# Performance work log

Measured on AMD Instinct MI355X. Metric: run time of the kernel, lower is better.

The kernel has to match this reference:

```python
import jax, jax.numpy as jnp
import numpy as np

EMBED_DIM = 1024
NUM_HEADS = 16
HEAD_DIM = EMBED_DIM // NUM_HEADS
BSZ, TGT, SRC = 4, 2048, 2048


def setup_inputs() -> dict:
    key = jax.random.key(0)
    ks = jax.random.split(key, 8)
    s = EMBED_DIM ** -0.5  # keep activations O(1)
    return {
        "query": jax.random.normal(ks[0], (BSZ, TGT, EMBED_DIM), jnp.float32),
        "key": jax.random.normal(ks[1], (BSZ, SRC, EMBED_DIM), jnp.float32),
        "key_padding_mask": jnp.ones((BSZ, SRC), jnp.float32),
        "Wq": jax.random.normal(ks[2], (EMBED_DIM, EMBED_DIM), jnp.float32) * s,
        "bq": jnp.zeros((EMBED_DIM,), jnp.float32),
        "Wk": jax.random.normal(ks[3], (EMBED_DIM, EMBED_DIM), jnp.float32) * s,
        "bk": jnp.zeros((EMBED_DIM,), jnp.float32),
        "Wv": jax.random.normal(ks[4], (EMBED_DIM, EMBED_DIM), jnp.float32) * s,
        "bv": jnp.zeros((EMBED_DIM,), jnp.float32),
        "Wo": jax.random.normal(ks[5], (EMBED_DIM, EMBED_DIM), jnp.float32) * s,
        "bo": jnp.zeros((EMBED_DIM,), jnp.float32),
    }


def _split_heads(x, bsz, seqlen):
    # [b, s, e] -> [b, h, s, d]
    return x.reshape(bsz, seqlen, NUM_HEADS, HEAD_DIM).transpose(0, 2, 1, 3)


def reference(query, key, key_padding_mask, Wq, bq, Wk, bk, Wv, bv, Wo, bo):
    bsz, src_len, embed_dim = key.shape
    tgt_len = query.shape[1]
    scaling = HEAD_DIM ** -0.5

    q = (query @ Wq.T + bq) * scaling                # [b, t, e]
    k = key @ Wk.T + bk                              # [b, s, e]
    v = key @ Wv.T + bv                              # [b, s, e]

    qh = _split_heads(q, bsz, tgt_len)               # [b, h, t, d]
    kh = _split_heads(k, bsz, src_len)               # [b, h, s, d]
    vh = _split_heads(v, bsz, src_len)               # [b, h, s, d]

    scores = jnp.einsum('bhtd,bhsd->bhts', qh, kh)   # [b, h, t, s]

    # _expand_mask: additive mask, 0 where mask==1, finfo.min where mask==0
    inv = 1.0 - key_padding_mask.astype(scores.dtype)
    neg = jnp.finfo(scores.dtype).min
    add_mask = jnp.where(inv.astype(bool), neg, inv)  # [b, s]
    scores = scores + add_mask[:, None, None, :]

    probs = jax.nn.softmax(scores, axis=-1)          # dropout p=0 / eval -> identity

    out = jnp.einsum('bhts,bhsd->bhtd', probs, vh)   # [b, h, t, d]
    out = out.transpose(0, 2, 1, 3).reshape(bsz, tgt_len, embed_dim)
    return out @ Wo.T + bo
```

## Files before the change

kernel.cpp:

```cpp
#include <hip/hip_runtime.h>

typedef unsigned short u16;
typedef __attribute__((ext_vector_type(8))) short bf16x8;
typedef __attribute__((ext_vector_type(4))) float f32x4;
typedef __attribute__((ext_vector_type(16))) float f32x16;

#define LOG2E 1.44269504088896f

__device__ inline u16 f2b(float f) {
  union { float f; unsigned u; } x; x.f = f;
  unsigned r = x.u + 0x7fffu + ((x.u >> 16) & 1u);
  return (u16)(r >> 16);
}

__device__ inline void gload_lds16(const void* g, void* l) {
  __builtin_amdgcn_global_load_lds(
      (__attribute__((address_space(1))) void*)(g),
      (__attribute__((address_space(3))) void*)(l), 16, 0, 0);
}

__device__ inline unsigned cvtpk_bf16(float lo, float hi_) {
  unsigned r;
  asm("v_cvt_pk_bf16_f32 %0, %1, %2" : "=v"(r) : "v"(lo), "v"(hi_));
  return r;
}
__device__ inline float exp2_hw(float x) { return __builtin_amdgcn_exp2f(x); }

__global__ __launch_bounds__(256) void cvt_all(
    const float* __restrict__ q, const float* __restrict__ k,
    const float* __restrict__ wq, const float* __restrict__ wk,
    const float* __restrict__ wv, const float* __restrict__ wo,
    u16* __restrict__ qb, u16* __restrict__ kb,
    u16* __restrict__ wqb, u16* __restrict__ wkb,
    u16* __restrict__ wvb, u16* __restrict__ wob) {
  int b = blockIdx.x;
  const float* in;
  u16* out;
  if (b < 8192) {
    in = q; out = qb;
  } else if (b < 16384) {
    in = k; out = kb; b -= 8192;
  } else {
    const int w = (b - 16384) >> 10;
    b = (b - 16384) & 1023;
    in = (w == 0) ? wq : (w == 1) ? wk : (w == 2) ? wv : wo;
    out = (w == 0) ? wqb : (w == 1) ? wkb : (w == 2) ? wvb : wob;
  }
  const int i = b * 256 + threadIdx.x;
  const float4 v = ((const float4*)in)[i];
  union { u16 s[4]; uint2 u; } o;
  o.s[0] = f2b(v.x); o.s[1] = f2b(v.y); o.s[2] = f2b(v.z); o.s[3] = f2b(v.w);
  ((uint2*)out)[i] = o.u;
}

template <int OUTMODE>
__global__ __launch_bounds__(256) void gemm_bt2(
    const u16* __restrict__ A, const u16* __restrict__ W,
    const float* __restrict__ bias, void* __restrict__ Cout,
    int M, int N, int K, float alpha) {
  __shared__ __align__(16) u16 lA[2][128 * 32];
  __shared__ __align__(16) u16 lW[2][128 * 32];
  const int tid = threadIdx.x, lane = tid & 63, wid = tid >> 6;
  const int wr = wid >> 1, wc = wid & 1;
  const int fr = lane & 15, fq = lane >> 4;
  const size_t abase = (size_t)blockIdx.x * 128 * K;
  const size_t wbase = (size_t)blockIdx.y * 128 * K;

  f32x4 acc[4][4];
#pragma unroll
  for (int i = 0; i < 4; ++i)
#pragma unroll
    for (int j = 0; j < 4; ++j) acc[i][j] = (f32x4){0.f, 0.f, 0.f, 0.f};

#define GSTAGE(bufi, kt)                                                          \
  do {                                                                            \
    _Pragma("unroll")                                                             \
    for (int is = 0; is < 2; ++is) {                                              \
      const int idx = is * 256 + tid;                                             \
      const int r = idx >> 2, c8 = (idx & 3) << 3;                                \
      gload_lds16(A + abase + (size_t)r * K + (kt) + c8, lA[bufi] + idx * 8);     \
      gload_lds16(W + wbase + (size_t)r * K + (kt) + c8, lW[bufi] + idx * 8);     \
    }                                                                             \
  } while (0)

  GSTAGE(0, 0);
  __syncthreads();

  int buf = 0;
  for (int kt = 0; kt < K; kt += 32) {
    if (kt + 32 < K) GSTAGE(buf ^ 1, kt + 32);
    bf16x8 af[4], wf[4];
#pragma unroll
    for (int m = 0; m < 4; ++m)
      af[m] = *(const bf16x8*)&lA[buf][(wr * 64 + m * 16 + fr) * 32 + fq * 8];
#pragma unroll
    for (int n = 0; n < 4; ++n)
      wf[n] = *(const bf16x8*)&lW[buf][(wc * 64 + n * 16 + fr) * 32 + fq * 8];
#pragma unroll
    for (int m = 0; m < 4; ++m)
#pragma unroll
      for (int n = 0; n < 4; ++n)
        acc[m][n] = __builtin_amdgcn_mfma_f32_16x16x32_bf16(af[m], wf[n], acc[m][n], 0, 0, 0);
    __syncthreads();
    buf ^= 1;
  }
#undef GSTAGE

  const int row0 = blockIdx.x * 128 + wr * 64 + fq * 4;
  const int col0 = blockIdx.y * 128 + wc * 64 + fr;
#pragma unroll
  for (int n = 0; n < 4; ++n) {
    const int col = col0 + n * 16;
    const float bb = bias[col];
#pragma unroll
    for (int m = 0; m < 4; ++m) {
#pragma unroll
      for (int r = 0; r < 4; ++r) {
        const int row = row0 + m * 16 + r;
        const float v = (acc[m][n][r] + bb) * alpha;
        if (OUTMODE == 1)
          ((float*)Cout)[(size_t)row * N + col] = v;
        else
          ((u16*)Cout)[(size_t)row * N + col] = f2b(v);
      }
    }
  }
}

__global__ __launch_bounds__(256) void gemm_kv(
    const u16* __restrict__ A, const u16* __restrict__ Wk,
    const u16* __restrict__ Wv, const float* __restrict__ bk,
    const float* __restrict__ bv, u16* __restrict__ Kout,
    u16* __restrict__ Vtout, int K) {
  __shared__ __align__(16) u16 lA[2][128 * 32];
  __shared__ __align__(16) u16 lW[2][128 * 32];
  const int tid = threadIdx.x, lane = tid & 63, wid = tid >> 6;
  const int wr = wid >> 1, wc = wid & 1;
  const int fr = lane & 15, fq = lane >> 4;
  const int isV = blockIdx.y >> 3, ny = blockIdx.y & 7;
  const u16* W = isV ? Wv : Wk;
  const float* bias = isV ? bv : bk;
  const size_t abase = (size_t)blockIdx.x * 128 * K;
  const size_t wbase = (size_t)ny * 128 * K;

  f32x4 acc[4][4];
#pragma unroll
  for (int i = 0; i < 4; ++i)
#pragma unroll
    for (int j = 0; j < 4; ++j) acc[i][j] = (f32x4){0.f, 0.f, 0.f, 0.f};

#define GSTAGE(bufi, kt)                                                          \
  do {                                                                            \
    _Pragma("unroll")                                                             \
    for (int is = 0; is < 2; ++is) {                                              \
      const int idx = is * 256 + tid;                                             \
      const int r = idx >> 2, c8 = (idx & 3) << 3;                                \
      gload_lds16(A + abase + (size_t)r * K + (kt) + c8, lA[bufi] + idx * 8);     \
      gload_lds16(W + wbase + (size_t)r * K + (kt) + c8, lW[bufi] + idx * 8);     \
    }                                                                             \
  } while (0)

  GSTAGE(0, 0);
  __syncthreads();

  int buf = 0;
  for (int kt = 0; kt < K; kt += 32) {
    if (kt + 32 < K) GSTAGE(buf ^ 1, kt + 32);
    bf16x8 af[4], wf[4];
#pragma unroll
    for (int m = 0; m < 4; ++m)
      af[m] = *(const bf16x8*)&lA[buf][(wr * 64 + m * 16 + fr) * 32 + fq * 8];
#pragma unroll
    for (int n = 0; n < 4; ++n)
      wf[n] = *(const bf16x8*)&lW[buf][(wc * 64 + n * 16 + fr) * 32 + fq * 8];
#pragma unroll
    for (int m = 0; m < 4; ++m)
#pragma unroll
      for (int n = 0; n < 4; ++n)
        acc[m][n] = __builtin_amdgcn_mfma_f32_16x16x32_bf16(af[m], wf[n], acc[m][n], 0, 0, 0);
    __syncthreads();
    buf ^= 1;
  }
#undef GSTAGE

  if (isV) {
    const int bI = blockIdx.x >> 4;
    const int srow0 = ((blockIdx.x * 128) & 2047) + wr * 64 + fq * 4;
    const int col0 = ny * 128 + wc * 64 + fr;
#pragma unroll
    for (int n = 0; n < 4; ++n) {
      const int col = col0 + n * 16;
      const float bb = bias[col];
      const int h = col >> 6, dl = col & 63;
      u16* vrow = Vtout + ((size_t)((bI * 16 + h) * 64 + dl)) * 2048;
#pragma unroll
      for (int m = 0; m < 4; ++m) {
        const int s = srow0 + m * 16;
        const int x = s & 15;
        const int pos = (((s & 63) >> 4) * 2 + ((x >> 2) & 1)) * 8 + ((x & 3) | ((x & 8) >> 1));
        union { u16 s4[4]; uint2 u; } w;
#pragma unroll
        for (int r = 0; r < 4; ++r) w.s4[r] = f2b(acc[m][n][r] + bb);
        *(uint2*)&vrow[(s >> 6) * 64 + pos] = w.u;
      }
    }
  } else {
    const int row0 = blockIdx.x * 128 + wr * 64 + fq * 4;
    const int col0 = ny * 128 + wc * 64 + fr;
#pragma unroll
    for (int n = 0; n < 4; ++n) {
      const int col = col0 + n * 16;
      const float bb = bias[col];
#pragma unroll
      for (int m = 0; m < 4; ++m) {
#pragma unroll
        for (int r = 0; r < 4; ++r) {
          const int row = row0 + m * 16 + r;
          Kout[(size_t)row * 1024 + col] = f2b(acc[m][n][r] + bb);
        }
      }
    }
  }
}

__global__ __launch_bounds__(512, 4) void flash16(
    const u16* __restrict__ Qb, const u16* __restrict__ Kb,
    const u16* __restrict__ Vt, const float* __restrict__ mask,
    u16* __restrict__ Ob) {
  __shared__ __align__(16) u16 Kl[2][4096];
  __shared__ __align__(16) u16 Vl[2][4096];
  __shared__ unsigned long long bml[32];
  __shared__ float lbuf[8][32];

  const int f = blockIdx.x;
  const int xcd = f & 7, i = f >> 3;
  const int bh = xcd * 8 + (i >> 3);
  const int qt = i & 7;
  const int b = bh >> 4, h = bh & 15;
  const int tid = threadIdx.x, lane = tid & 63, wid = tid >> 6;
  const int l31 = lane & 31, hi = lane >> 5;
  const int qrow0 = qt * 256 + wid * 32;

  bf16x8 qf[4];
  {
    const u16* qp = Qb + ((size_t)(b * 2048 + qrow0 + l31)) * 1024 + h * 64;
#pragma unroll
    for (int dc = 0; dc < 4; ++dc) qf[dc] = *(const bf16x8*)(qp + dc * 16 + hi * 8);
  }

  const u16* kbase = Kb + ((size_t)(b * 2048)) * 1024 + h * 64;
  const u16* vbase = Vt + ((size_t)(bh * 64)) * 2048;
  const float* mrow = mask + b * 2048;

  const int l31s = tid & 31, his = (tid >> 5) & 1, mid = (tid >> 6) & 3,
            top = (tid >> 8) & 1;
  const int koff = (top * 32 + l31s) * 1024 + (mid * 2 + his) * 8;
  const int voff = (top * 32 + l31s) * 2048 + (mid * 2 + his) * 8;

  f32x16 o0 = {}, o1 = {};
  float l_r = 0.f;

#define STAGE(bufi, tt)                               \
  do {                                                \
    const u16* kb_t = kbase + (size_t)(tt) * 65536;   \
    const u16* vb_t = vbase + (tt) * 64;              \
    gload_lds16(kb_t + koff, &Kl[bufi][tid * 8]);     \
    gload_lds16(vb_t + voff, &Vl[bufi][tid * 8]);     \
  } while (0)

  STAGE(0, 0);

#pragma unroll
  for (int tt = 0; tt < 4; ++tt) {
    const int tile = wid * 4 + tt;
    const unsigned long long bmv = __ballot(mrow[tile * 64 + lane] == 1.0f);
    if (lane == 0) bml[tile] = bmv;
  }
  __syncthreads();

  const unsigned mflags =
      (unsigned)__ballot(lane < 32 && bml[lane] != ~0ull);

  for (int t = 0; t < 32; ++t) {
    const int cur = t & 1;
    if (t + 1 < 32) STAGE(cur ^ 1, t + 1);

    const u16* Kc = Kl[cur];
    const u16* Vc = Vl[cur];

#pragma unroll
    for (int n = 0; n < 2; ++n) {
      f32x16 acc = {};
#pragma unroll
      for (int dc = 0; dc < 4; ++dc) {
        const bf16x8 kf = *(const bf16x8*)&Kc[(n * 4 + dc) * 512 + lane * 8];
        acc = __builtin_amdgcn_mfma_f32_32x32x16_bf16(kf, qf[dc], acc, 0, 0, 0);
      }

#pragma unroll
      for (int reg = 0; reg < 16; ++reg) acc[reg] = exp2_hw(acc[reg]);

      if (mflags & (1u << t)) {
        const unsigned long long bm = bml[t];
#pragma unroll
        for (int reg = 0; reg < 16; ++reg) {
          const int k = n * 32 + (reg & 3) + 8 * (reg >> 2) + 4 * hi;
          if (!((bm >> k) & 1)) acc[reg] = 0.f;
        }
      }

      {
        float s0a = (acc[0] + acc[1]) + (acc[2] + acc[3]);
        float s1a = (acc[4] + acc[5]) + (acc[6] + acc[7]);
        float s2a = (acc[8] + acc[9]) + (acc[10] + acc[11]);
        float s3a = (acc[12] + acc[13]) + (acc[14] + acc[15]);
        l_r += (s0a + s1a) + (s2a + s3a);
      }

      bf16x8 pa0, pa1;
      {
        union { unsigned u[4]; bf16x8 v; } pk;
#pragma unroll
        for (int j = 0; j < 4; ++j) pk.u[j] = cvtpk_bf16(acc[2 * j], acc[2 * j + 1]);
        pa0 = pk.v;
#pragma unroll
        for (int j = 0; j < 4; ++j) pk.u[j] = cvtpk_bf16(acc[8 + 2 * j], acc[9 + 2 * j]);
        pa1 = pk.v;
      }

      {
        const bf16x8 v00 = *(const bf16x8*)&Vc[(0 * 4 + n * 2 + 0) * 512 + lane * 8];
        const bf16x8 v01 = *(const bf16x8*)&Vc[(0 * 4 + n * 2 + 1) * 512 + lane * 8];
        o0 = __builtin_amdgcn_mfma_f32_32x32x16_bf16(pa0, v00, o0, 0, 0, 0);
        o0 = __builtin_amdgcn_mfma_f32_32x32x16_bf16(pa1, v01, o0, 0, 0, 0);
      }
      {
        const bf16x8 v10 = *(const bf16x8*)&Vc[(1 * 4 + n * 2 + 0) * 512 + lane * 8];
        const bf16x8 v11 = *(const bf16x8*)&Vc[(1 * 4 + n * 2 + 1) * 512 + lane * 8];
        o1 = __builtin_amdgcn_mfma_f32_32x32x16_bf16(pa0, v10, o1, 0, 0, 0);
        o1 = __builtin_amdgcn_mfma_f32_32x32x16_bf16(pa1, v11, o1, 0, 0, 0);
      }
    }

    __syncthreads();
  }
#undef STAGE

  const float l_tot = l_r + __shfl_xor(l_r, 32);
  const float linv = 1.0f / l_tot;
  if (!hi) lbuf[wid][l31] = linv;
  __builtin_amdgcn_wave_barrier();
  float lv[16];
#pragma unroll
  for (int reg = 0; reg < 16; ++reg)
    lv[reg] = lbuf[wid][(reg & 3) + 8 * (reg >> 2) + 4 * hi];

  u16* ob = Ob + ((size_t)(b * 2048 + qrow0)) * 1024 + h * 64 + l31;
#pragma unroll
  for (int reg = 0; reg < 16; ++reg) {
    const int q = (reg & 3) + 8 * (reg >> 2) + 4 * hi;
    ob[(size_t)q * 1024] = f2b(o0[reg] * lv[reg]);
    ob[(size_t)q * 1024 + 32] = f2b(o1[reg] * lv[reg]);
  }
}

extern "C" void kernel_launch(void* const* d_in, const int* in_sizes, int n_in,
                              void* d_out, int out_size, void* d_ws, size_t ws_size,
                              hipStream_t stream) {
  const float* query = (const float*)d_in[0];
  const float* keyin = (const float*)d_in[1];
  const float* maskp = (const float*)d_in[2];
  const float* Wq = (const float*)d_in[3];
  const float* bq = (const float*)d_in[4];
  const float* Wk = (const float*)d_in[5];
  const float* bk = (const float*)d_in[6];
  const float* Wv = (const float*)d_in[7];
  const float* bv = (const float*)d_in[8];
  const float* Wo = (const float*)d_in[9];
  const float* bo = (const float*)d_in[10];

  char* ws = (char*)d_ws;
  const size_t ACT = (size_t)8192 * 1024 * 2;
  const size_t WMAT = (size_t)1024 * 1024 * 2;
  u16* qbf = (u16*)(ws);
  u16* kbf = (u16*)(ws + ACT);
  u16* wqb = (u16*)(ws + 2 * ACT);
  u16* wkb = (u16*)(ws + 2 * ACT + WMAT);
  u16* wvb = (u16*)(ws + 2 * ACT + 2 * WMAT);
  u16* wob = (u16*)(ws + 2 * ACT + 3 * WMAT);
  u16* Qb  = (u16*)(ws + 2 * ACT + 4 * WMAT);
  u16* Kb  = (u16*)(ws + 3 * ACT + 4 * WMAT);
  u16* Vt = qbf;
  u16* attnb = kbf;

  cvt_all<<<20480, 256, 0, stream>>>(query, keyin, Wq, Wk, Wv, Wo,
                                     qbf, kbf, wqb, wkb, wvb, wob);

  dim3 gg(64, 8);
  gemm_bt2<0><<<gg, 256, 0, stream>>>(qbf, wqb, bq, Qb, 8192, 1024, 1024, 0.125f * LOG2E);
  gemm_kv<<<dim3(64, 16), 256, 0, stream>>>(kbf, wkb, wvb, bk, bv, Kb, Vt, 1024);

  flash16<<<512, 512, 0, stream>>>(Qb, Kb, Vt, maskp, attnb);

  gemm_bt2<1><<<gg, 256, 0, stream>>>(attnb, wob, bo, d_out, 8192, 1024, 1024, 1.0f);
}
```

Measured before the change: 203.6 us.

## Fuse Q, K, V projections into one launch and deepen GEMM K-tile to 64

Merges the separate Q projection GEMM and the K/V GEMM into a single 64x24-block launch that picks its input, weight, bias and output per blockIdx.y. Vt now goes to a dedicated workspace region because qbf is still being read by the Q blocks in the same launch. Both GEMMs now stage 64-wide K slices (double-buffered, 64 KB LDS), which halves the barrier count per tile. The cost is more LDS per block, which may lower occupancy, and the workspace must be large enough for the extra buffer.

```diff
diff --git a/kernel.cpp b/kernel.cpp
--- a/kernel.cpp
+++ b/kernel.cpp
@@ -53,13 +53,12 @@
   ((uint2*)out)[i] = o.u;
 }
 
-template <int OUTMODE>
-__global__ __launch_bounds__(256) void gemm_bt2(
+__global__ __launch_bounds__(256) void gemm_o(
     const u16* __restrict__ A, const u16* __restrict__ W,
-    const float* __restrict__ bias, void* __restrict__ Cout,
-    int M, int N, int K, float alpha) {
-  __shared__ __align__(16) u16 lA[2][128 * 32];
-  __shared__ __align__(16) u16 lW[2][128 * 32];
+    const float* __restrict__ bias, float* __restrict__ Cout,
+    int K) {
+  __shared__ __align__(16) u16 lA[2][128 * 64];
+  __shared__ __align__(16) u16 lW[2][128 * 64];
   const int tid = threadIdx.x, lane = tid & 63, wid = tid >> 6;
   const int wr = wid >> 1, wc = wid & 1;
   const int fr = lane & 15, fq = lane >> 4;
@@ -75,11 +74,11 @@
 #define GSTAGE(bufi, kt)                                                          \
   do {                                                                            \
     _Pragma("unroll")                                                             \
-    for (int is = 0; is < 2; ++is) {                                              \
-      const int idx = is * 256 + tid;                                             \
-      const int r = idx >> 2, c8 = (idx & 3) << 3;                                \
-      gload_lds16(A + abase + (size_t)r * K + (kt) + c8, lA[bufi] + idx * 8);     \
-      gload_lds16(W + wbase + (size_t)r * K + (kt) + c8, lW[bufi] + idx * 8);     \
+    for (int is = 0; is < 4; ++is) {                                              \
+      const int c = is * 256 + tid;                                               \
+      const int r = c >> 3, c8 = (c & 7) << 3;                                    \
+      gload_lds16(A + abase + (size_t)r * K + (kt) + c8, lA[bufi] + c * 8);       \
+      gload_lds16(W + wbase + (size_t)r * K + (kt) + c8, lW[bufi] + c * 8);       \
     }                                                                             \
   } while (0)
 
@@ -87,20 +86,23 @@
   __syncthreads();
 
   int buf = 0;
-  for (int kt = 0; kt < K; kt += 32) {
-    if (kt + 32 < K) GSTAGE(buf ^ 1, kt + 32);
-    bf16x8 af[4], wf[4];
-#pragma unroll
-    for (int m = 0; m < 4; ++m)
-      af[m] = *(const bf16x8*)&lA[buf][(wr * 64 + m * 16 + fr) * 32 + fq * 8];
-#pragma unroll
-    for (int n = 0; n < 4; ++n)
-      wf[n] = *(const bf16x8*)&lW[buf][(wc * 64 + n * 16 + fr) * 32 + fq * 8];
-#pragma unroll
-    for (int m = 0; m < 4; ++m)
+  for (int kt = 0; kt < K; kt += 64) {
+    if (kt + 64 < K) GSTAGE(buf ^ 1, kt + 64);
+#pragma unroll
+    for (int kk = 0; kk < 2; ++kk) {
+      bf16x8 af[4], wf[4];
+#pragma unroll
+      for (int m = 0; m < 4; ++m)
+        af[m] = *(const bf16x8*)&lA[buf][(wr * 64 + m * 16 + fr) * 64 + kk * 32 + fq * 8];
 #pragma unroll
       for (int n = 0; n < 4; ++n)
-        acc[m][n] = __builtin_amdgcn_mfma_f32_16x16x32_bf16(af[m], wf[n], acc[m][n], 0, 0, 0);
+        wf[n] = *(const bf16x8*)&lW[buf][(wc * 64 + n * 16 + fr) * 64 + kk * 32 + fq * 8];
+#pragma unroll
+      for (int m = 0; m < 4; ++m)
+#pragma unroll
+        for (int n = 0; n < 4; ++n)
+          acc[m][n] = __builtin_amdgcn_mfma_f32_16x16x32_bf16(af[m], wf[n], acc[m][n], 0, 0, 0);
+    }
     __syncthreads();
     buf ^= 1;
   }
@@ -117,29 +119,28 @@
 #pragma unroll
       for (int r = 0; r < 4; ++r) {
         const int row = row0 + m * 16 + r;
-        const float v = (acc[m][n][r] + bb) * alpha;
-        if (OUTMODE == 1)
-          ((float*)Cout)[(size_t)row * N + col] = v;
-        else
-          ((u16*)Cout)[(size_t)row * N + col] = f2b(v);
-      }
-    }
-  }
-}
-
-__global__ __launch_bounds__(256) void gemm_kv(
-    const u16* __restrict__ A, const u16* __restrict__ Wk,
-    const u16* __restrict__ Wv, const float* __restrict__ bk,
-    const float* __restrict__ bv, u16* __restrict__ Kout,
+        Cout[(size_t)row * 1024 + col] = acc[m][n][r] + bb;
+      }
+    }
+  }
+}
+
+__global__ __launch_bounds__(256) void gemm_qkv(
+    const u16* __restrict__ qA, const u16* __restrict__ kA,
+    const u16* __restrict__ Wq, const u16* __restrict__ Wk,
+    const u16* __restrict__ Wv, const float* __restrict__ bq,
+    const float* __restrict__ bk, const float* __restrict__ bv,
+    u16* __restrict__ Qout, u16* __restrict__ Kout,
     u16* __restrict__ Vtout, int K) {
-  __shared__ __align__(16) u16 lA[2][128 * 32];
-  __shared__ __align__(16) u16 lW[2][128 * 32];
+  __shared__ __align__(16) u16 lA[2][128 * 64];
+  __shared__ __align__(16) u16 lW[2][128 * 64];
   const int tid = threadIdx.x, lane = tid & 63, wid = tid >> 6;
   const int wr = wid >> 1, wc = wid & 1;
   const int fr = lane & 15, fq = lane >> 4;
-  const int isV = blockIdx.y >> 3, ny = blockIdx.y & 7;
-  const u16* W = isV ? Wv : Wk;
-  const float* bias = isV ? bv : bk;
+  const int path = blockIdx.y >> 3, ny = blockIdx.y & 7;
+  const u16* A = (path == 0) ? qA : kA;
+  const u16* W = (path == 0) ? Wq : (path == 1) ? Wk : Wv;
+  const float* bias = (path == 0) ? bq : (path == 1) ? bk : bv;
   const size_t abase = (size_t)blockIdx.x * 128 * K;
   const size_t wbase = (size_t)ny * 128 * K;
 
@@ -152,11 +153,11 @@
 #define GSTAGE(bufi, kt)                                                          \
   do {                                                                            \
     _Pragma("unroll")                                                             \
-    for (int is = 0; is < 2; ++is) {                                              \
-      const int idx = is * 256 + tid;                                             \
-      const int r = idx >> 2, c8 = (idx & 3) << 3;                                \
-      gload_lds16(A + abase + (size_t)r * K + (kt) + c8, lA[bufi] + idx * 8);     \
-      gload_lds16(W + wbase + (size_t)r * K + (kt) + c8, lW[bufi] + idx * 8);     \
+    for (int is = 0; is < 4; ++is) {                                              \
+      const int c = is * 256 + tid;                                               \
+      const int r = c >> 3, c8 = (c & 7) << 3;                                    \
+      gload_lds16(A + abase + (size_t)r * K + (kt) + c8, lA[bufi] + c * 8);       \
+      gload_lds16(W + wbase + (size_t)r * K + (kt) + c8, lW[bufi] + c * 8);       \
     }                                                                             \
   } while (0)
 
@@ -164,26 +165,29 @@
   __syncthreads();
 
   int buf = 0;
-  for (int kt = 0; kt < K; kt += 32) {
-    if (kt + 32 < K) GSTAGE(buf ^ 1, kt + 32);
-    bf16x8 af[4], wf[4];
-#pragma unroll
-    for (int m = 0; m < 4; ++m)
-      af[m] = *(const bf16x8*)&lA[buf][(wr * 64 + m * 16 + fr) * 32 + fq * 8];
-#pragma unroll
-    for (int n = 0; n < 4; ++n)
-      wf[n] = *(const bf16x8*)&lW[buf][(wc * 64 + n * 16 + fr) * 32 + fq * 8];
-#pragma unroll
-    for (int m = 0; m < 4; ++m)
+  for (int kt = 0; kt < K; kt += 64) {
+    if (kt + 64 < K) GSTAGE(buf ^ 1, kt + 64);
+#pragma unroll
+    for (int kk = 0; kk < 2; ++kk) {
+      bf16x8 af[4], wf[4];
+#pragma unroll
+      for (int m = 0; m < 4; ++m)
+        af[m] = *(const bf16x8*)&lA[buf][(wr * 64 + m * 16 + fr) * 64 + kk * 32 + fq * 8];
 #pragma unroll
       for (int n = 0; n < 4; ++n)
-        acc[m][n] = __builtin_amdgcn_mfma_f32_16x16x32_bf16(af[m], wf[n], acc[m][n], 0, 0, 0);
+        wf[n] = *(const bf16x8*)&lW[buf][(wc * 64 + n * 16 + fr) * 64 + kk * 32 + fq * 8];
+#pragma unroll
+      for (int m = 0; m < 4; ++m)
+#pragma unroll
+        for (int n = 0; n < 4; ++n)
+          acc[m][n] = __builtin_amdgcn_mfma_f32_16x16x32_bf16(af[m], wf[n], acc[m][n], 0, 0, 0);
+    }
     __syncthreads();
     buf ^= 1;
   }
 #undef GSTAGE
 
-  if (isV) {
+  if (path == 2) {
     const int bI = blockIdx.x >> 4;
     const int srow0 = ((blockIdx.x * 128) & 2047) + wr * 64 + fq * 4;
     const int col0 = ny * 128 + wc * 64 + fr;
@@ -205,6 +209,8 @@
       }
     }
   } else {
+    const float alpha = (path == 0) ? 0.125f * LOG2E : 1.0f;
+    u16* Cout = (path == 0) ? Qout : Kout;
     const int row0 = blockIdx.x * 128 + wr * 64 + fq * 4;
     const int col0 = ny * 128 + wc * 64 + fr;
 #pragma unroll
@@ -216,7 +222,7 @@
 #pragma unroll
         for (int r = 0; r < 4; ++r) {
           const int row = row0 + m * 16 + r;
-          Kout[(size_t)row * 1024 + col] = f2b(acc[m][n][r] + bb);
+          Cout[(size_t)row * 1024 + col] = f2b((acc[m][n][r] + bb) * alpha);
         }
       }
     }
@@ -396,11 +402,12 @@
   cvt_all<<<20480, 256, 0, stream>>>(query, keyin, Wq, Wk, Wv, Wo,
                                      qbf, kbf, wqb, wkb, wvb, wob);
 
-  dim3 gg(64, 8);
-  gemm_bt2<0><<<gg, 256, 0, stream>>>(qbf, wqb, bq, Qb, 8192, 1024, 1024, 0.125f * LOG2E);
-  gemm_kv<<<dim3(64, 16), 256, 0, stream>>>(kbf, wkb, wvb, bk, bv, Kb, Vt, 1024);
-
-  flash16<<<512, 512, 0, stream>>>(Qb, Kb, Vt, maskp, attnb);
-
-  gemm_bt2<1><<<gg, 256, 0, stream>>>(attnb, wob, bo, d_out, 8192, 1024, 1024, 1.0f);
-}
+  u16* VtDed = (u16*)(ws + 4 * ACT + 4 * WMAT);
+
+  gemm_qkv<<<dim3(64, 24), 256, 0, stream>>>(qbf, kbf, wqb, wkb, wvb,
+                                             bq, bk, bv, Qb, Kb, VtDed, 1024);
+
+  flash16<<<512, 512, 0, stream>>>(Qb, Kb, VtDed, maskp, attnb);
+
+  gemm_o<<<dim3(64, 8), 256, 0, stream>>>(attnb, wob, bo, (float*)d_out, 1024);
+}
```

Result: no change. 206.0 us (+1.2%).
